# Kernel optimization log

Hardware: AMD Instinct MI355X
Metric: run time of the kernel (lower is better)

The kernel has to match this reference:

```python
import jax, jax.numpy as jnp
import numpy as np

B, C, D, H = 128, 8, 1024, 8
K_RANGE = (2, 3, 4, 5)


def setup_inputs() -> dict:
    key = jax.random.key(0)
    ks = jax.random.split(key, 10)
    s = 0.02
    return {
        "x": jax.random.normal(ks[0], (B, D), jnp.float32),
        # per-K prototype groups, shape (nb_classes, K, embed_dim) as in get_prototype_group()
        "p2": jax.random.normal(ks[1], (C, 2, D), jnp.float32),
        "p3": jax.random.normal(ks[2], (C, 3, D), jnp.float32),
        "p4": jax.random.normal(ks[3], (C, 4, D), jnp.float32),
        "p5": jax.random.normal(ks[4], (C, 5, D), jnp.float32),
        # per-class attention Block params (stacked over class axis)
        "ln_g": jnp.ones((C, D), jnp.float32),
        "ln_b": jnp.zeros((C, D), jnp.float32),
        "w_qkv": jax.random.normal(ks[5], (C, 3 * D, D), jnp.float32) * s,
        "b_qkv": jnp.zeros((C, 3 * D), jnp.float32),
        "w_proj": jax.random.normal(ks[6], (C, D, D), jnp.float32) * s,
        "b_proj": jnp.zeros((C, D), jnp.float32),
        # cls head
        "w_cls": jax.random.normal(ks[7], (C, D), jnp.float32) * s,
        "b_cls": jnp.zeros((C,), jnp.float32),
    }


def _proto_group(x, pg):
    """x: (B,D); pg: (C,K,D). Returns nearest proto (B,D), per-sample class group (B,K,D), class ids (B,)."""
    Cc, K, d = pg.shape
    flat = pg.reshape(Cc * K, d)
    # squared L2 distances (argmin identical to torch.cdist p=2 argmin)
    d2 = (jnp.sum(x * x, axis=1, keepdims=True)
          - 2.0 * (x @ flat.T)
          + jnp.sum(flat * flat, axis=1))
    idx = jnp.argmin(d2, axis=1)          # (B,)
    cls = idx // K                        # (B,)
    return flat[idx], pg[cls], cls


def _vicreg(x, nearest, proto_space, sim_c=25.0, std_c=25.0, cov_c=1.0):
    # sim: pull x toward its nearest prototype in every K-group
    repr_loss = jnp.mean((x[:, None, :] - nearest) ** 2)
    # std over batch of prototype space, unbiased var, eps=1e-4
    std = jnp.sqrt(jnp.var(proto_space, axis=0, ddof=1) + 1e-4)   # (S,D)
    std_loss = jnp.mean(jax.nn.relu(1.0 - std))
    # covariance of centered flattened prototype space
    ps = proto_space - jnp.mean(proto_space, axis=0)
    P = ps.reshape(-1, ps.shape[-1])                              # (B*S, D)
    cov = P.T @ P / (P.shape[0] - 1)
    cov_loss = ((cov ** 2).sum() - (jnp.diagonal(cov) ** 2).sum()) / ps.shape[-1]
    return sim_c * repr_loss + std_c * std_loss + cov_c * cov_loss


def _forward(x, p2, p3, p4, p5, ln_g, ln_b, w_qkv, b_qkv, w_proj, b_proj, w_cls, b_cls):
    groups = (p2, p3, p4, p5)
    nearest_list, space_list, cls = [], [], None
    for pg in groups:
        n, sp, cls = _proto_group(x, pg)   # cls kept from LAST group, as in torch code
        nearest_list.append(n)
        space_list.append(sp)
    nearest = jnp.stack(nearest_list, axis=1)     # (B, len(K_range), D)
    proto_space = jnp.concatenate(space_list, 1)  # (B, sum(K_range), D)

    vcr = _vicreg(x, nearest, proto_space)

    # per-class attention Block: LayerNorm -> MHA -> residual, vectorized over class axis c
    S = proto_space.shape[1]
    mu = proto_space.mean(-1, keepdims=True)
    var = proto_space.var(-1, keepdims=True)
    xn = (proto_space - mu) * jax.lax.rsqrt(var + 1e-5)               # (B,S,D)
    h = xn[None] * ln_g[:, None, None, :] + ln_b[:, None, None, :]    # (C,B,S,D)

    qkv = jnp.einsum('cbsd,cfd->cbsf', h, w_qkv) + b_qkv[:, None, None, :]
    dh = D // H
    qkv = qkv.reshape(C, B, S, 3, H, dh).transpose(3, 0, 1, 4, 2, 5)  # (3,C,B,H,S,dh)
    q, k, v = qkv[0] * (dh ** -0.5), qkv[1], qkv[2]
    attn = jax.nn.softmax(jnp.einsum('cbhqe,cbhke->cbhqk', q, k), axis=-1)
    o = jnp.einsum('cbhqk,cbhke->cbhqe', attn, v)                     # (C,B,H,S,dh)
    o = o.transpose(0, 1, 3, 2, 4).reshape(C, B, S, D)
    out = jnp.einsum('cbsd,ced->cbse', o, w_proj) + b_proj[:, None, None, :]
    attended = proto_space[None] + out                                # (C,B,S,D)

    # route each sample through the block of its (last-group) assigned class
    cond = attended[cls, jnp.arange(B)]                               # (B,S,D)
    cond = cond / jnp.maximum(jnp.linalg.norm(cond, axis=2, keepdims=True), 1e-12)
    pooled = cond.mean(1)                                             # (B,D)
    logits = pooled @ w_cls.T + b_cls
    return logits, vcr


def reference(x, p2, p3, p4, p5, ln_g, ln_b, w_qkv, b_qkv, w_proj, b_proj, w_cls, b_cls):
    return _forward(x, p2, p3, p4, p5, ln_g, ln_b, w_qkv, b_qkv, w_proj, b_proj, w_cls, b_cls)
```

## Files before the change

kernel.cpp:

```cpp
#include <hip/hip_runtime.h>
#include <math.h>

#define NB 128
#define ND 1024
#define NS 14
#define NDH 128

typedef float f32x4 __attribute__((ext_vector_type(4)));
typedef short bf16x8 __attribute__((ext_vector_type(8)));

__device__ __forceinline__ unsigned short f2bf(float v) {
  unsigned int u = __builtin_bit_cast(unsigned int, v);
  return (unsigned short)((u + 0x7FFFu + ((u >> 16) & 1u)) >> 16);
}
__device__ __forceinline__ float bf2f(unsigned short u) {
  return __builtin_bit_cast(float, (unsigned int)u << 16);
}

__device__ __forceinline__ void gl_lds16(const void* g, void* l) {
  __builtin_amdgcn_global_load_lds(
      (const __attribute__((address_space(1))) void*)g,
      (__attribute__((address_space(3))) void*)l, 16, 0, 0);
}

__device__ __forceinline__ void s_decomp(int s, int& g, int& k) {
  if (s < 2)      { g = 0; k = s; }
  else if (s < 5) { g = 1; k = s - 2; }
  else if (s < 9) { g = 2; k = s - 5; }
  else            { g = 3; k = s - 9; }
}
__device__ __forceinline__ const float* grp_ptr(int g, const float* p2, const float* p3,
                                                const float* p4, const float* p5) {
  return g == 0 ? p2 : g == 1 ? p3 : g == 2 ? p4 : p5;
}
__device__ __forceinline__ int grp_base(int g) { return g == 0 ? 0 : g == 1 ? 16 : g == 2 ? 40 : 72; }
__device__ __forceinline__ int grp_k(int g) { return g + 2; }

__global__ __launch_bounds__(256) void k_assign_ln(
    const float* __restrict__ x,
    const float* __restrict__ p2, const float* __restrict__ p3,
    const float* __restrict__ p4, const float* __restrict__ p5,
    const float* __restrict__ ln_g, const float* __restrict__ ln_b,
    unsigned short* __restrict__ hbf, float* __restrict__ pall,
    int* __restrict__ cls, int* __restrict__ rows_g, float* __restrict__ minv)
{
  int bid = blockIdx.x, t = threadIdx.x;
  __shared__ __align__(16) float xs[ND];
  float4* xs4 = (float4*)xs;
  if (bid < 112) {
    int r = bid;
    const float* pp; int idx;
    if (r < 16)      { pp = p2; idx = r; }
    else if (r < 40) { pp = p3; idx = r - 16; }
    else if (r < 72) { pp = p4; idx = r - 40; }
    else             { pp = p5; idx = r - 72; }
    const float4* row4 = (const float4*)(pp + (size_t)idx * ND);
    float4 v = row4[t];
    xs4[t] = v;
    float s1 = v.x + v.y + v.z + v.w;
    float s2 = v.x * v.x + v.y * v.y + v.z * v.z + v.w * v.w;
    __shared__ float ra[256], rb[256];
    ra[t] = s1; rb[t] = s2; __syncthreads();
    for (int o = 128; o > 0; o >>= 1) { if (t < o) { ra[t] += ra[t + o]; rb[t] += rb[t + o]; } __syncthreads(); }
    __shared__ float mu, rstd;
    if (t == 0) {
      float m = ra[0] * (1.f / 1024.f);
      float var = rb[0] * (1.f / 1024.f) - m * m;
      mu = m; rstd = rsqrtf(var + 1e-5f);
    }
    __syncthreads();
    ((float4*)(pall + (size_t)r * ND))[t] = xs4[t];
    float4 xv = xs4[t];
    float nx = (xv.x - mu) * rstd, ny = (xv.y - mu) * rstd,
          nz = (xv.z - mu) * rstd, nw = (xv.w - mu) * rstd;
#pragma unroll
    for (int c = 0; c < 8; ++c) {
      float4 g = ((const float4*)(ln_g + (size_t)c * ND))[t];
      float4 bb = ((const float4*)(ln_b + (size_t)c * ND))[t];
      ushort4 u;
      u.x = f2bf(nx * g.x + bb.x); u.y = f2bf(ny * g.y + bb.y);
      u.z = f2bf(nz * g.z + bb.z); u.w = f2bf(nw * g.w + bb.w);
      ((ushort4*)(hbf + ((size_t)(c * 112 + r)) * ND))[t] = u;
    }
  } else {
    int b = bid - 112;
    __shared__ float d2s[112];
    __shared__ int cls_s[4];
    const float4* xg4 = (const float4*)(x + (size_t)b * ND);
    xs4[t] = xg4[t];
    __syncthreads();
    if (t < 112) {
      const float* pp; int idx;
      if (t < 16)      { pp = p2; idx = t; }
      else if (t < 40) { pp = p3; idx = t - 16; }
      else if (t < 72) { pp = p4; idx = t - 40; }
      else             { pp = p5; idx = t - 72; }
      const float4* pr4 = (const float4*)(pp + (size_t)idx * ND);
      float acc = 0.f;
#pragma unroll 8
      for (int d = 0; d < 256; ++d) {
        float4 a = xs4[d], p = pr4[d];
        float dx = a.x - p.x, dy = a.y - p.y, dz = a.z - p.z, dw = a.w - p.w;
        acc += dx * dx + dy * dy + dz * dz + dw * dw;
      }
      d2s[t] = acc;
    }
    __syncthreads();
    if (t < 4) {
      int base = grp_base(t), kg = grp_k(t), cnt = 8 * kg;
      float mv = d2s[base]; int mi = 0;
      for (int j = 1; j < cnt; ++j) { float v = d2s[base + j]; if (v < mv) { mv = v; mi = j; } }
      int c = mi / kg;
      cls[b * 4 + t] = c; cls_s[t] = c;
      minv[b * 4 + t] = mv;
    }
    __syncthreads();
    if (t < NS) {
      int g, k; s_decomp(t, g, k);
      rows_g[b * NS + t] = grp_base(g) + cls_s[g] * grp_k(g) + k;
    }
  }
}

__global__ __launch_bounds__(128) void k_prep(
    const int* __restrict__ cls, const float* __restrict__ minv,
    int* __restrict__ counts, int* __restrict__ ccnt, int* __restrict__ order,
    float* __restrict__ scal)
{
  __shared__ int cnt_s[32];
  __shared__ int cc_s[8];
  __shared__ float red[128];
  int t = threadIdx.x;
  if (t < 32) cnt_s[t] = 0;
  if (t < 8) cc_s[t] = 0;
  if (t < 4) scal[t] = 0.f;
  __syncthreads();
  int c3;
#pragma unroll
  for (int g = 0; g < 4; ++g) {
    int c = cls[t * 4 + g];
    atomicAdd(&cnt_s[g * 8 + c], 1);
    if (g == 3) c3 = c;
  }
  int pos = atomicAdd(&cc_s[c3], 1);
  order[c3 * 128 + pos] = t;
  red[t] = minv[t * 4 + 0] + minv[t * 4 + 1] + minv[t * 4 + 2] + minv[t * 4 + 3];
  __syncthreads();
  for (int o = 64; o > 0; o >>= 1) { if (t < o) red[t] += red[t + o]; __syncthreads(); }
  if (t == 0) scal[0] = red[0];
  if (t < 32) counts[t] = cnt_s[t];
  if (t < 8) ccnt[t] = cc_s[t];
}

__global__ __launch_bounds__(256) void k_stats(
    const float* __restrict__ p2, const float* __restrict__ p3,
    const float* __restrict__ p4, const float* __restrict__ p5,
    const int* __restrict__ counts, float* __restrict__ M, float* __restrict__ scal)
{
  int idx = blockIdx.x * 256 + threadIdx.x;
  int s = idx >> 10, d = idx & 1023;
  int g, k; s_decomp(s, g, k);
  const float* pp = grp_ptr(g, p2, p3, p4, p5);
  int kg = grp_k(g);
  float vc[8], nc[8];
  float sum = 0.f, sumsq = 0.f;
#pragma unroll
  for (int c = 0; c < 8; ++c) {
    float v = pp[((size_t)(c * kg + k)) * ND + d];
    float n = (float)counts[g * 8 + c];
    vc[c] = v; nc[c] = n;
    sum += n * v; sumsq += n * v * v;
  }
  float mean = sum * (1.f / 128.f);
  float var = (sumsq - 128.f * mean * mean) * (1.f / 127.f);
  float sd = sqrtf(var + 1e-4f);
#pragma unroll
  for (int c = 0; c < 8; ++c)
    M[((size_t)(s * 8 + c)) * ND + d] = sqrtf(nc[c] * (1.f / 1791.f)) * (vc[c] - mean);
  float part = fmaxf(1.f - sd, 0.f);
  __shared__ float red[256];
  red[threadIdx.x] = part; __syncthreads();
  for (int o = 128; o > 0; o >>= 1) { if (threadIdx.x < o) red[threadIdx.x] += red[threadIdx.x + o]; __syncthreads(); }
  if (threadIdx.x == 0) atomicAdd(&scal[1], red[0]);
}

__global__ __launch_bounds__(128) void k_gramdiag(const float* __restrict__ M, float* __restrict__ scal)
{
  __shared__ float mi[ND];
  __shared__ float red[128];
  int bid = blockIdx.x, t = threadIdx.x;
  if (bid < 112) {
    for (int d = t; d < ND; d += 128) mi[d] = M[(size_t)bid * ND + d];
    __syncthreads();
    float p = 0.f;
    if (t < 112) {
      const float* mj = M + (size_t)t * ND;
      float acc = 0.f;
      for (int d = 0; d < ND; ++d) acc += mi[d] * mj[d];
      p = acc * acc;
    }
    red[t] = p; __syncthreads();
    for (int o = 64; o > 0; o >>= 1) { if (t < o) red[t] += red[t + o]; __syncthreads(); }
    if (t == 0) atomicAdd(&scal[2], red[0]);
  } else {
    int d = (bid - 112) * 128 + t;
    float tsum = 0.f;
    for (int r = 0; r < 112; ++r) { float v = M[(size_t)r * ND + d]; tsum += v * v; }
    red[t] = tsum * tsum; __syncthreads();
    for (int o = 64; o > 0; o >>= 1) { if (t < o) red[t] += red[t + o]; __syncthreads(); }
    if (t == 0) atomicAdd(&scal[3], red[0]);
  }
}

__global__ __launch_bounds__(128) void k_qkv_mfma(
    const unsigned short* __restrict__ hbf, const float* __restrict__ w_qkv,
    const float* __restrict__ b_qkv, unsigned short* __restrict__ qkv_bf)
{
  __shared__ __align__(16) float Wl[32 * 128];
  __shared__ __align__(16) unsigned short Hl[112 * 128];
  int c = blockIdx.y;
  int nb0 = blockIdx.x * 32;
  int t = threadIdx.x, lane = t & 63, wv = t >> 6;
  const float* W = w_qkv + ((size_t)c * 3072 + nb0) * ND;
  const unsigned short* H = hbf + (size_t)c * 112 * ND;

  const char* wsrc[8]; char* wdst[8];
#pragma unroll
  for (int j = 0; j < 8; ++j) {
    int n = (wv * 8 + j) * 2 + (lane >> 5);
    int cbs = ((lane & 31) * 16) ^ ((n & 15) << 5);
    wsrc[j] = (const char*)(W + (size_t)n * ND) + cbs;
    wdst[j] = (char*)Wl + (wv * 8 + j) * 1024;
  }
  const char* hsrc[14]; char* hdst[14];
#pragma unroll
  for (int j = 0; j < 14; ++j) {
    int r = (wv * 14 + j) * 4 + (lane >> 4);
    int cbs = ((lane & 15) * 16) ^ ((r & 15) << 4);
    hsrc[j] = (const char*)(H + (size_t)r * ND) + cbs;
    hdst[j] = (char*)Hl + (wv * 14 + j) * 1024;
  }

  f32x4 acc[7] = {};
  int r16 = lane & 15, q = lane >> 4;
  const char* wrow = (const char*)Wl + (wv * 16 + r16) * 512;
  int swq = r16 << 5, swa = r16 << 4;

  for (int kt = 0; kt < ND; kt += 128) {
    __syncthreads();
#pragma unroll
    for (int j = 0; j < 8; ++j) gl_lds16(wsrc[j] + (size_t)kt * 4, wdst[j]);
#pragma unroll
    for (int j = 0; j < 14; ++j) gl_lds16(hsrc[j] + (size_t)kt * 2, hdst[j]);
    __syncthreads();
#pragma unroll
    for (int kk4 = 0; kk4 < 4; ++kk4) {
      int o = (kk4 * 128 + q * 32) ^ swq;
      float4 w0 = *(const float4*)(wrow + o);
      float4 w1 = *(const float4*)(wrow + o + 16);
      bf16x8 bv;
      bv[0] = (short)f2bf(w0.x); bv[1] = (short)f2bf(w0.y);
      bv[2] = (short)f2bf(w0.z); bv[3] = (short)f2bf(w0.w);
      bv[4] = (short)f2bf(w1.x); bv[5] = (short)f2bf(w1.y);
      bv[6] = (short)f2bf(w1.z); bv[7] = (short)f2bf(w1.w);
      int oa = (kk4 * 64 + q * 16) ^ swa;
#pragma unroll
      for (int m = 0; m < 7; ++m) {
        bf16x8 av = *(const bf16x8*)((const char*)Hl + (m * 16 + r16) * 256 + oa);
        acc[m] = __builtin_amdgcn_mfma_f32_16x16x32_bf16(av, bv, acc[m], 0, 0, 0);
      }
    }
  }
  int col = nb0 + wv * 16 + r16;
  float bq = b_qkv[(size_t)c * 3072 + col];
  int rbase = q * 4;
#pragma unroll
  for (int m = 0; m < 7; ++m)
#pragma unroll
    for (int r = 0; r < 4; ++r)
      qkv_bf[((size_t)c * 112 + m * 16 + rbase + r) * 3072 + col] = f2bf(acc[m][r] + bq);
}

__global__ __launch_bounds__(256) void k_attn(
    const unsigned short* __restrict__ qkv_bf, const int* __restrict__ cls,
    const int* __restrict__ rows_g, unsigned short* __restrict__ obf)
{
  __shared__ __align__(16) float qs[NS * NDH], ks2[NS * NDH], vs[NS * NDH];
  __shared__ float sc[NS * NS];
  __shared__ int rg[NS];
  int h = blockIdx.x, b = blockIdx.y, t = threadIdx.x;
  if (t < NS) rg[t] = rows_g[b * NS + t];
  __syncthreads();
  int cp = cls[b * 4 + 3];
  const float scale = 0.08838834764831843f;
  for (int i = t; i < NS * 64; i += 256) {
    int s = i >> 6, e2 = (i & 63) * 2;
    size_t base = ((size_t)cp * 112 + rg[s]) * 3072 + h * NDH + e2;
    unsigned int uq = *(const unsigned int*)&qkv_bf[base];
    unsigned int uk = *(const unsigned int*)&qkv_bf[base + 1024];
    unsigned int uv = *(const unsigned int*)&qkv_bf[base + 2048];
    qs[s * NDH + e2]      = bf2f((unsigned short)uq) * scale;
    qs[s * NDH + e2 + 1]  = bf2f((unsigned short)(uq >> 16)) * scale;
    ks2[s * NDH + e2]     = bf2f((unsigned short)uk);
    ks2[s * NDH + e2 + 1] = bf2f((unsigned short)(uk >> 16));
    vs[s * NDH + e2]      = bf2f((unsigned short)uv);
    vs[s * NDH + e2 + 1]  = bf2f((unsigned short)(uv >> 16));
  }
  __syncthreads();
  if (t < NS * NS) {
    int si = t / NS, sj = t - (t / NS) * NS;
    const float4* qa = (const float4*)&qs[si * NDH];
    const float4* kb = (const float4*)&ks2[sj * NDH];
    float acc = 0.f;
#pragma unroll 8
    for (int e4 = 0; e4 < 32; ++e4) {
      float4 a = qa[e4], k4 = kb[e4];
      acc += a.x * k4.x + a.y * k4.y + a.z * k4.z + a.w * k4.w;
    }
    sc[t] = acc;
  }
  __syncthreads();
  if (t < NS) {
    float m = -1e30f;
    for (int j = 0; j < NS; ++j) m = fmaxf(m, sc[t * NS + j]);
    float e_[NS]; float sum = 0.f;
    for (int j = 0; j < NS; ++j) { float e = expf(sc[t * NS + j] - m); e_[j] = e; sum += e; }
    float inv = 1.f / sum;
    for (int j = 0; j < NS; ++j) sc[t * NS + j] = e_[j] * inv;
  }
  __syncthreads();
  for (int i = t; i < NS * 32; i += 256) {
    int s = i >> 5, e4 = i & 31;
    float4 a = {0.f, 0.f, 0.f, 0.f};
#pragma unroll
    for (int j = 0; j < NS; ++j) {
      float w = sc[s * NS + j];
      float4 v4 = ((const float4*)&vs[j * NDH])[e4];
      a.x += w * v4.x; a.y += w * v4.y; a.z += w * v4.z; a.w += w * v4.w;
    }
    ushort4 u; u.x = f2bf(a.x); u.y = f2bf(a.y); u.z = f2bf(a.z); u.w = f2bf(a.w);
    ((ushort4*)&obf[((size_t)b * NS + s) * ND + h * NDH])[e4] = u;
  }
}

__global__ __launch_bounds__(256) void k_proj_mfma(
    const unsigned short* __restrict__ obf, const int* __restrict__ order,
    const int* __restrict__ ccnt, const int* __restrict__ rows_g,
    const float* __restrict__ w_proj, const float* __restrict__ b_proj,
    const float* __restrict__ pall, float* __restrict__ att)
{
  int c = blockIdx.y >> 3, ch = blockIdx.y & 7;
  int cnt = ccnt[c];
  int nb = cnt - ch * 16;
  if (nb <= 0) return;
  if (nb > 16) nb = 16;
  __shared__ __align__(16) float Wl[32 * 128];
  __shared__ __align__(16) unsigned short Al[224 * 128];
  __shared__ int sid_s[16];
  int t = threadIdx.x, lane = t & 63, wv = t >> 6;
  if (t < 16) sid_s[t] = order[c * 128 + ch * 16 + ((t < nb) ? t : 0)];
  __syncthreads();
  int nb0 = blockIdx.x * 32;
  const float* W = w_proj + ((size_t)c * ND + nb0) * ND;

  const char* wsrc[4]; char* wdst[4];
#pragma unroll
  for (int j = 0; j < 4; ++j) {
    int n = (wv * 4 + j) * 2 + (lane >> 5);
    int cbs = ((lane & 31) * 16) ^ ((n & 15) << 5);
    wsrc[j] = (const char*)(W + (size_t)n * ND) + cbs;
    wdst[j] = (char*)Wl + (wv * 4 + j) * 1024;
  }
  const char* asrc[14]; char* adst[14];
#pragma unroll
  for (int j = 0; j < 14; ++j) {
    int r = (wv * 14 + j) * 4 + (lane >> 4);
    int cbs = ((lane & 15) * 16) ^ ((r & 15) << 4);
    int si = r / 14, s = r - si * 14;
    asrc[j] = (const char*)(obf + ((size_t)sid_s[si] * NS + s) * ND) + cbs;
    adst[j] = (char*)Al + (wv * 14 + j) * 1024;
  }

  f32x4 acc[7] = {};
  int r16 = lane & 15, q = lane >> 4;
  int colh = wv & 1, rowh = wv >> 1;
  const char* wrow = (const char*)Wl + (colh * 16 + r16) * 512;
  int swq = r16 << 5, swa = r16 << 4;

  for (int kt = 0; kt < ND; kt += 128) {
    __syncthreads();
#pragma unroll
    for (int j = 0; j < 4; ++j) gl_lds16(wsrc[j] + (size_t)kt * 4, wdst[j]);
#pragma unroll
    for (int j = 0; j < 14; ++j) gl_lds16(asrc[j] + (size_t)kt * 2, adst[j]);
    __syncthreads();
#pragma unroll
    for (int kk4 = 0; kk4 < 4; ++kk4) {
      int o = (kk4 * 128 + q * 32) ^ swq;
      float4 w0 = *(const float4*)(wrow + o);
      float4 w1 = *(const float4*)(wrow + o + 16);
      bf16x8 bv;
      bv[0] = (short)f2bf(w0.x); bv[1] = (short)f2bf(w0.y);
      bv[2] = (short)f2bf(w0.z); bv[3] = (short)f2bf(w0.w);
      bv[4] = (short)f2bf(w1.x); bv[5] = (short)f2bf(w1.y);
      bv[6] = (short)f2bf(w1.z); bv[7] = (short)f2bf(w1.w);
      int oa = (kk4 * 64 + q * 16) ^ swa;
#pragma unroll
      for (int m = 0; m < 7; ++m) {
        int row = rowh * 112 + m * 16 + r16;
        bf16x8 av = *(const bf16x8*)((const char*)Al + row * 256 + oa);
        acc[m] = __builtin_amdgcn_mfma_f32_16x16x32_bf16(av, bv, acc[m], 0, 0, 0);
      }
    }
  }
  int col = nb0 + colh * 16 + r16;
  float bp = b_proj[(size_t)c * ND + col];
  int rbase = q * 4;
#pragma unroll
  for (int m = 0; m < 7; ++m)
#pragma unroll
    for (int r = 0; r < 4; ++r) {
      int row = rowh * 112 + m * 16 + rbase + r;
      int si = row / 14, s = row - si * 14;
      if (si < nb) {
        int b = sid_s[si];
        float res = pall[(size_t)rows_g[b * NS + s] * ND + col];
        att[((size_t)b * NS + s) * ND + col] = acc[m][r] + bp + res;
      }
    }
}

__global__ __launch_bounds__(256) void k_final(
    const float* __restrict__ att, const float* __restrict__ w_cls,
    const float* __restrict__ b_cls, const float* __restrict__ scal,
    float* __restrict__ out)
{
  int b = blockIdx.x, t = threadIdx.x;
  __shared__ __align__(16) float as[NS * ND];
  __shared__ float wred[NS][4];
  __shared__ float inv[NS];
  __shared__ __align__(16) float pooled[ND];
  int lane = t & 63, w = t >> 6;
#pragma unroll
  for (int s = 0; s < NS; ++s) {
    float4 v = ((const float4*)(att + ((size_t)b * NS + s) * ND))[t];
    ((float4*)&as[s * ND])[t] = v;
    float p = v.x * v.x + v.y * v.y + v.z * v.z + v.w * v.w;
#pragma unroll
    for (int o = 32; o > 0; o >>= 1) p += __shfl_xor(p, o, 64);
    if (lane == 0) wred[s][w] = p;
  }
  __syncthreads();
  if (t < NS) {
    float s2 = wred[t][0] + wred[t][1] + wred[t][2] + wred[t][3];
    inv[t] = 1.f / fmaxf(sqrtf(s2), 1e-12f);
  }
  __syncthreads();
  float4 pa = {0.f, 0.f, 0.f, 0.f};
#pragma unroll
  for (int s = 0; s < NS; ++s) {
    float iv = inv[s];
    float4 v = ((const float4*)&as[s * ND])[t];
    pa.x += iv * v.x; pa.y += iv * v.y; pa.z += iv * v.z; pa.w += iv * v.w;
  }
  const float k14 = 1.f / 14.f;
  pa.x *= k14; pa.y *= k14; pa.z *= k14; pa.w *= k14;
  ((float4*)pooled)[t] = pa;
  __syncthreads();
  int c = t >> 5, l = t & 31;
  float acc = 0.f;
#pragma unroll
  for (int k = 0; k < 8; ++k) {
    int i4 = l + k * 32;
    float4 p4 = ((const float4*)pooled)[i4];
    float4 wc = ((const float4*)(w_cls + (size_t)c * ND))[i4];
    acc += p4.x * wc.x + p4.y * wc.y + p4.z * wc.z + p4.w * wc.w;
  }
  for (int o = 16; o > 0; o >>= 1) acc += __shfl_down(acc, o, 32);
  if (l == 0) out[b * 8 + c] = acc + b_cls[c];
  if (b == 0 && t == 0) {
    float repr = scal[0] * (1.f / (128.f * 4.f * 1024.f));
    float stdl = scal[1] * (1.f / 14336.f);
    float covl = (scal[2] - scal[3]) * (1.f / 1024.f);
    out[1024] = 25.f * repr + 25.f * stdl + covl;
  }
}

extern "C" void kernel_launch(void* const* d_in, const int* in_sizes, int n_in,
                              void* d_out, int out_size, void* d_ws, size_t ws_size,
                              hipStream_t stream) {
  const float* x      = (const float*)d_in[0];
  const float* p2     = (const float*)d_in[1];
  const float* p3     = (const float*)d_in[2];
  const float* p4     = (const float*)d_in[3];
  const float* p5     = (const float*)d_in[4];
  const float* ln_g   = (const float*)d_in[5];
  const float* ln_b   = (const float*)d_in[6];
  const float* w_qkv  = (const float*)d_in[7];
  const float* b_qkv  = (const float*)d_in[8];
  const float* w_proj = (const float*)d_in[9];
  const float* b_proj = (const float*)d_in[10];
  const float* w_cls  = (const float*)d_in[11];
  const float* b_cls  = (const float*)d_in[12];
  float* out = (float*)d_out;
  char* ws = (char*)d_ws;

  float* scal   = (float*)(ws + 0);
  int*   counts = (int*)(ws + 64);
  int*   ccnt   = (int*)(ws + 192);
  int*   cls    = (int*)(ws + 256);
  int*   rows_g = (int*)(ws + 2304);
  int*   order  = (int*)(ws + 9472);
  float* minv   = (float*)(ws + 13568);
  float* pall   = (float*)(ws + 16384);
  unsigned short* hbf  = (unsigned short*)(ws + 475136);
  unsigned short* qkvb = (unsigned short*)(ws + 2310144);
  unsigned short* obf  = (unsigned short*)(ws + 9191424);
  float* att    = (float*)(ws + 12861440);
  float* M      = (float*)(ws + 20201472);

  k_assign_ln<<<240, 256, 0, stream>>>(x, p2, p3, p4, p5, ln_g, ln_b, hbf, pall, cls, rows_g, minv);
  k_qkv_mfma<<<dim3(96, 8), 128, 0, stream>>>(hbf, w_qkv, b_qkv, qkvb);
  k_prep<<<1, 128, 0, stream>>>(cls, minv, counts, ccnt, order, scal);
  k_stats<<<56, 256, 0, stream>>>(p2, p3, p4, p5, counts, M, scal);
  k_gramdiag<<<120, 128, 0, stream>>>(M, scal);
  k_attn<<<dim3(8, 128), 256, 0, stream>>>(qkvb, cls, rows_g, obf);
  k_proj_mfma<<<dim3(32, 64), 256, 0, stream>>>(obf, order, ccnt, rows_g, w_proj, b_proj, pall, att);
  k_final<<<128, 256, 0, stream>>>(att, w_cls, b_cls, scal, out);
}
```

Measured before the change: 136.0 us.

## Store GEMM operands in MFMA fragment order and load directly from global memory

The LayerNorm output and the attention output are now written in a pre-swizzled layout that matches the MFMA 16x16x32 operand fragment order. This lets the QKV and projection GEMMs drop LDS staging and barriers and read operands straight from global/L2. The projection kernel now computes 64 output columns per block with 14 accumulators, halving the grid, and weight conversion uses the packed bf16 convert instruction. k_gramdiag also gets float4 vectorized loads. The trade-off is the loss of explicit LDS reuse, relying on cache for operands that are reread across blocks and waves, plus higher register pressure.

```diff
diff --git a/kernel.cpp b/kernel.cpp
--- a/kernel.cpp
+++ b/kernel.cpp
@@ -8,6 +8,7 @@
 
 typedef float f32x4 __attribute__((ext_vector_type(4)));
 typedef short bf16x8 __attribute__((ext_vector_type(8)));
+typedef unsigned int u32x4 __attribute__((ext_vector_type(4)));
 
 __device__ __forceinline__ unsigned short f2bf(float v) {
   unsigned int u = __builtin_bit_cast(unsigned int, v);
@@ -17,10 +18,14 @@
   return __builtin_bit_cast(float, (unsigned int)u << 16);
 }
 
-__device__ __forceinline__ void gl_lds16(const void* g, void* l) {
-  __builtin_amdgcn_global_load_lds(
-      (const __attribute__((address_space(1))) void*)g,
-      (__attribute__((address_space(3))) void*)l, 16, 0, 0);
+__device__ __forceinline__ bf16x8 pack_bv(float4 w0, float4 w1) {
+  unsigned int u0, u1, u2, u3;
+  asm("v_cvt_pk_bf16_f32 %0, %1, %2" : "=v"(u0) : "v"(w0.x), "v"(w0.y));
+  asm("v_cvt_pk_bf16_f32 %0, %1, %2" : "=v"(u1) : "v"(w0.z), "v"(w0.w));
+  asm("v_cvt_pk_bf16_f32 %0, %1, %2" : "=v"(u2) : "v"(w1.x), "v"(w1.y));
+  asm("v_cvt_pk_bf16_f32 %0, %1, %2" : "=v"(u3) : "v"(w1.z), "v"(w1.w));
+  u32x4 u = {u0, u1, u2, u3};
+  return __builtin_bit_cast(bf16x8, u);
 }
 
 __device__ __forceinline__ void s_decomp(int s, int& g, int& k) {
@@ -41,7 +46,7 @@
     const float* __restrict__ p2, const float* __restrict__ p3,
     const float* __restrict__ p4, const float* __restrict__ p5,
     const float* __restrict__ ln_g, const float* __restrict__ ln_b,
-    unsigned short* __restrict__ hbf, float* __restrict__ pall,
+    unsigned short* __restrict__ hbf2, float* __restrict__ pall,
     int* __restrict__ cls, int* __restrict__ rows_g, float* __restrict__ minv)
 {
   int bid = blockIdx.x, t = threadIdx.x;
@@ -73,6 +78,10 @@
     float4 xv = xs4[t];
     float nx = (xv.x - mu) * rstd, ny = (xv.y - mu) * rstd,
           nz = (xv.z - mu) * rstd, nw = (xv.w - mu) * rstd;
+    int d0 = t * 4;
+    int m = r >> 4, rr = r & 15;
+    int kblk = d0 >> 5, qq = (d0 >> 3) & 3, e0 = d0 & 7;
+    size_t fidx = (((size_t)kblk * 7 + m) * 64 + qq * 16 + rr) * 8 + e0;
 #pragma unroll
     for (int c = 0; c < 8; ++c) {
       float4 g = ((const float4*)(ln_g + (size_t)c * ND))[t];
@@ -80,7 +89,7 @@
       ushort4 u;
       u.x = f2bf(nx * g.x + bb.x); u.y = f2bf(ny * g.y + bb.y);
       u.z = f2bf(nz * g.z + bb.z); u.w = f2bf(nw * g.w + bb.w);
-      ((ushort4*)(hbf + ((size_t)(c * 112 + r)) * ND))[t] = u;
+      *(ushort4*)&hbf2[(size_t)c * 114688 + fidx] = u;
     }
   } else {
     int b = bid - 112;
@@ -186,17 +195,23 @@
 
 __global__ __launch_bounds__(128) void k_gramdiag(const float* __restrict__ M, float* __restrict__ scal)
 {
-  __shared__ float mi[ND];
+  __shared__ __align__(16) float mi[ND];
   __shared__ float red[128];
   int bid = blockIdx.x, t = threadIdx.x;
   if (bid < 112) {
-    for (int d = t; d < ND; d += 128) mi[d] = M[(size_t)bid * ND + d];
+    float4* mi4 = (float4*)mi;
+    const float4* src4 = (const float4*)(M + (size_t)bid * ND);
+    for (int d = t; d < 256; d += 128) mi4[d] = src4[d];
     __syncthreads();
     float p = 0.f;
     if (t < 112) {
-      const float* mj = M + (size_t)t * ND;
+      const float4* mj4 = (const float4*)(M + (size_t)t * ND);
       float acc = 0.f;
-      for (int d = 0; d < ND; ++d) acc += mi[d] * mj[d];
+#pragma unroll 8
+      for (int d = 0; d < 256; ++d) {
+        float4 a = mi4[d], b = mj4[d];
+        acc += a.x * b.x + a.y * b.y + a.z * b.z + a.w * b.w;
+      }
       p = acc * acc;
     }
     red[t] = p; __syncthreads();
@@ -213,65 +228,28 @@
 }
 
 __global__ __launch_bounds__(128) void k_qkv_mfma(
-    const unsigned short* __restrict__ hbf, const float* __restrict__ w_qkv,
+    const unsigned short* __restrict__ hbf2, const float* __restrict__ w_qkv,
     const float* __restrict__ b_qkv, unsigned short* __restrict__ qkv_bf)
 {
-  __shared__ __align__(16) float Wl[32 * 128];
-  __shared__ __align__(16) unsigned short Hl[112 * 128];
   int c = blockIdx.y;
-  int nb0 = blockIdx.x * 32;
   int t = threadIdx.x, lane = t & 63, wv = t >> 6;
-  const float* W = w_qkv + ((size_t)c * 3072 + nb0) * ND;
-  const unsigned short* H = hbf + (size_t)c * 112 * ND;
-
-  const char* wsrc[8]; char* wdst[8];
-#pragma unroll
-  for (int j = 0; j < 8; ++j) {
-    int n = (wv * 8 + j) * 2 + (lane >> 5);
-    int cbs = ((lane & 31) * 16) ^ ((n & 15) << 5);
-    wsrc[j] = (const char*)(W + (size_t)n * ND) + cbs;
-    wdst[j] = (char*)Wl + (wv * 8 + j) * 1024;
-  }
-  const char* hsrc[14]; char* hdst[14];
-#pragma unroll
-  for (int j = 0; j < 14; ++j) {
-    int r = (wv * 14 + j) * 4 + (lane >> 4);
-    int cbs = ((lane & 15) * 16) ^ ((r & 15) << 4);
-    hsrc[j] = (const char*)(H + (size_t)r * ND) + cbs;
-    hdst[j] = (char*)Hl + (wv * 14 + j) * 1024;
-  }
-
+  int r16 = lane & 15, q = lane >> 4;
+  int col = blockIdx.x * 32 + wv * 16 + r16;
+  const float* Wp = w_qkv + ((size_t)c * 3072 + col) * ND + q * 8;
+  const unsigned short* Hp = hbf2 + (size_t)c * 114688 + lane * 8;
   f32x4 acc[7] = {};
-  int r16 = lane & 15, q = lane >> 4;
-  const char* wrow = (const char*)Wl + (wv * 16 + r16) * 512;
-  int swq = r16 << 5, swa = r16 << 4;
-
-  for (int kt = 0; kt < ND; kt += 128) {
-    __syncthreads();
-#pragma unroll
-    for (int j = 0; j < 8; ++j) gl_lds16(wsrc[j] + (size_t)kt * 4, wdst[j]);
-#pragma unroll
-    for (int j = 0; j < 14; ++j) gl_lds16(hsrc[j] + (size_t)kt * 2, hdst[j]);
-    __syncthreads();
-#pragma unroll
-    for (int kk4 = 0; kk4 < 4; ++kk4) {
-      int o = (kk4 * 128 + q * 32) ^ swq;
-      float4 w0 = *(const float4*)(wrow + o);
-      float4 w1 = *(const float4*)(wrow + o + 16);
-      bf16x8 bv;
-      bv[0] = (short)f2bf(w0.x); bv[1] = (short)f2bf(w0.y);
-      bv[2] = (short)f2bf(w0.z); bv[3] = (short)f2bf(w0.w);
-      bv[4] = (short)f2bf(w1.x); bv[5] = (short)f2bf(w1.y);
-      bv[6] = (short)f2bf(w1.z); bv[7] = (short)f2bf(w1.w);
-      int oa = (kk4 * 64 + q * 16) ^ swa;
-#pragma unroll
-      for (int m = 0; m < 7; ++m) {
-        bf16x8 av = *(const bf16x8*)((const char*)Hl + (m * 16 + r16) * 256 + oa);
-        acc[m] = __builtin_amdgcn_mfma_f32_16x16x32_bf16(av, bv, acc[m], 0, 0, 0);
-      }
-    }
-  }
-  int col = nb0 + wv * 16 + r16;
+#pragma unroll 2
+  for (int kb = 0; kb < 32; ++kb) {
+    float4 w0 = *(const float4*)(Wp + kb * 32);
+    float4 w1 = *(const float4*)(Wp + kb * 32 + 4);
+    bf16x8 bv = pack_bv(w0, w1);
+    const unsigned short* hk = Hp + kb * 3584;
+#pragma unroll
+    for (int m = 0; m < 7; ++m) {
+      bf16x8 av = *(const bf16x8*)(hk + m * 512);
+      acc[m] = __builtin_amdgcn_mfma_f32_16x16x32_bf16(av, bv, acc[m], 0, 0, 0);
+    }
+  }
   float bq = b_qkv[(size_t)c * 3072 + col];
   int rbase = q * 4;
 #pragma unroll
@@ -283,7 +261,7 @@
 
 __global__ __launch_bounds__(256) void k_attn(
     const unsigned short* __restrict__ qkv_bf, const int* __restrict__ cls,
-    const int* __restrict__ rows_g, unsigned short* __restrict__ obf)
+    const int* __restrict__ rows_g, unsigned short* __restrict__ obf2)
 {
   __shared__ __align__(16) float qs[NS * NDH], ks2[NS * NDH], vs[NS * NDH];
   __shared__ float sc[NS * NS];
@@ -338,13 +316,15 @@
       float4 v4 = ((const float4*)&vs[j * NDH])[e4];
       a.x += w * v4.x; a.y += w * v4.y; a.z += w * v4.z; a.w += w * v4.w;
     }
+    int d = h * NDH + e4 * 4;
+    int kblk = d >> 5, qq = (d >> 3) & 3, e0 = d & 7;
     ushort4 u; u.x = f2bf(a.x); u.y = f2bf(a.y); u.z = f2bf(a.z); u.w = f2bf(a.w);
-    ((ushort4*)&obf[((size_t)b * NS + s) * ND + h * NDH])[e4] = u;
+    *(ushort4*)&obf2[(size_t)b * 14336 + kblk * 448 + s * 32 + qq * 8 + e0] = u;
   }
 }
 
 __global__ __launch_bounds__(256) void k_proj_mfma(
-    const unsigned short* __restrict__ obf, const int* __restrict__ order,
+    const unsigned short* __restrict__ obf2, const int* __restrict__ order,
     const int* __restrict__ ccnt, const int* __restrict__ rows_g,
     const float* __restrict__ w_proj, const float* __restrict__ b_proj,
     const float* __restrict__ pall, float* __restrict__ att)
@@ -354,73 +334,40 @@
   int nb = cnt - ch * 16;
   if (nb <= 0) return;
   if (nb > 16) nb = 16;
-  __shared__ __align__(16) float Wl[32 * 128];
-  __shared__ __align__(16) unsigned short Al[224 * 128];
   __shared__ int sid_s[16];
   int t = threadIdx.x, lane = t & 63, wv = t >> 6;
   if (t < 16) sid_s[t] = order[c * 128 + ch * 16 + ((t < nb) ? t : 0)];
   __syncthreads();
-  int nb0 = blockIdx.x * 32;
-  const float* W = w_proj + ((size_t)c * ND + nb0) * ND;
-
-  const char* wsrc[4]; char* wdst[4];
-#pragma unroll
-  for (int j = 0; j < 4; ++j) {
-    int n = (wv * 4 + j) * 2 + (lane >> 5);
-    int cbs = ((lane & 31) * 16) ^ ((n & 15) << 5);
-    wsrc[j] = (const char*)(W + (size_t)n * ND) + cbs;
-    wdst[j] = (char*)Wl + (wv * 4 + j) * 1024;
-  }
-  const char* asrc[14]; char* adst[14];
-#pragma unroll
-  for (int j = 0; j < 14; ++j) {
-    int r = (wv * 14 + j) * 4 + (lane >> 4);
-    int cbs = ((lane & 15) * 16) ^ ((r & 15) << 4);
-    int si = r / 14, s = r - si * 14;
-    asrc[j] = (const char*)(obf + ((size_t)sid_s[si] * NS + s) * ND) + cbs;
-    adst[j] = (char*)Al + (wv * 14 + j) * 1024;
-  }
-
-  f32x4 acc[7] = {};
   int r16 = lane & 15, q = lane >> 4;
-  int colh = wv & 1, rowh = wv >> 1;
-  const char* wrow = (const char*)Wl + (colh * 16 + r16) * 512;
-  int swq = r16 << 5, swa = r16 << 4;
-
-  for (int kt = 0; kt < ND; kt += 128) {
-    __syncthreads();
-#pragma unroll
-    for (int j = 0; j < 4; ++j) gl_lds16(wsrc[j] + (size_t)kt * 4, wdst[j]);
-#pragma unroll
-    for (int j = 0; j < 14; ++j) gl_lds16(asrc[j] + (size_t)kt * 2, adst[j]);
-    __syncthreads();
-#pragma unroll
-    for (int kk4 = 0; kk4 < 4; ++kk4) {
-      int o = (kk4 * 128 + q * 32) ^ swq;
-      float4 w0 = *(const float4*)(wrow + o);
-      float4 w1 = *(const float4*)(wrow + o + 16);
-      bf16x8 bv;
-      bv[0] = (short)f2bf(w0.x); bv[1] = (short)f2bf(w0.y);
-      bv[2] = (short)f2bf(w0.z); bv[3] = (short)f2bf(w0.w);
-      bv[4] = (short)f2bf(w1.x); bv[5] = (short)f2bf(w1.y);
-      bv[6] = (short)f2bf(w1.z); bv[7] = (short)f2bf(w1.w);
-      int oa = (kk4 * 64 + q * 16) ^ swa;
-#pragma unroll
-      for (int m = 0; m < 7; ++m) {
-        int row = rowh * 112 + m * 16 + r16;
-        bf16x8 av = *(const bf16x8*)((const char*)Al + row * 256 + oa);
-        acc[m] = __builtin_amdgcn_mfma_f32_16x16x32_bf16(av, bv, acc[m], 0, 0, 0);
-      }
-    }
-  }
-  int col = nb0 + colh * 16 + r16;
+  int col = blockIdx.x * 64 + wv * 16 + r16;
+  const float* Wp = w_proj + ((size_t)c * ND + col) * ND + q * 8;
+  const unsigned short* ap[14];
+#pragma unroll
+  for (int m = 0; m < 14; ++m) {
+    int row = m * 16 + r16;
+    int si = row / 14, s = row - si * 14;
+    ap[m] = obf2 + (size_t)sid_s[si] * 14336 + s * 32 + q * 8;
+  }
+  f32x4 acc[14] = {};
+#pragma unroll 2
+  for (int kb = 0; kb < 32; ++kb) {
+    float4 w0 = *(const float4*)(Wp + kb * 32);
+    float4 w1 = *(const float4*)(Wp + kb * 32 + 4);
+    bf16x8 bv = pack_bv(w0, w1);
+    int ko = kb * 448;
+#pragma unroll
+    for (int m = 0; m < 14; ++m) {
+      bf16x8 av = *(const bf16x8*)(ap[m] + ko);
+      acc[m] = __builtin_amdgcn_mfma_f32_16x16x32_bf16(av, bv, acc[m], 0, 0, 0);
+    }
+  }
   float bp = b_proj[(size_t)c * ND + col];
   int rbase = q * 4;
 #pragma unroll
-  for (int m = 0; m < 7; ++m)
+  for (int m = 0; m < 14; ++m)
 #pragma unroll
     for (int r = 0; r < 4; ++r) {
-      int row = rowh * 112 + m * 16 + rbase + r;
+      int row = m * 16 + rbase + r;
       int si = row / 14, s = row - si * 14;
       if (si < nb) {
         int b = sid_s[si];
@@ -513,18 +460,18 @@
   int*   order  = (int*)(ws + 9472);
   float* minv   = (float*)(ws + 13568);
   float* pall   = (float*)(ws + 16384);
-  unsigned short* hbf  = (unsigned short*)(ws + 475136);
+  unsigned short* hbf2 = (unsigned short*)(ws + 475136);
   unsigned short* qkvb = (unsigned short*)(ws + 2310144);
-  unsigned short* obf  = (unsigned short*)(ws + 9191424);
+  unsigned short* obf2 = (unsigned short*)(ws + 9191424);
   float* att    = (float*)(ws + 12861440);
   float* M      = (float*)(ws + 20201472);
 
-  k_assign_ln<<<240, 256, 0, stream>>>(x, p2, p3, p4, p5, ln_g, ln_b, hbf, pall, cls, rows_g, minv);
-  k_qkv_mfma<<<dim3(96, 8), 128, 0, stream>>>(hbf, w_qkv, b_qkv, qkvb);
+  k_assign_ln<<<240, 256, 0, stream>>>(x, p2, p3, p4, p5, ln_g, ln_b, hbf2, pall, cls, rows_g, minv);
+  k_qkv_mfma<<<dim3(96, 8), 128, 0, stream>>>(hbf2, w_qkv, b_qkv, qkvb);
   k_prep<<<1, 128, 0, stream>>>(cls, minv, counts, ccnt, order, scal);
   k_stats<<<56, 256, 0, stream>>>(p2, p3, p4, p5, counts, M, scal);
   k_gramdiag<<<120, 128, 0, stream>>>(M, scal);
-  k_attn<<<dim3(8, 128), 256, 0, stream>>>(qkvb, cls, rows_g, obf);
-  k_proj_mfma<<<dim3(32, 64), 256, 0, stream>>>(obf, order, ccnt, rows_g, w_proj, b_proj, pall, att);
+  k_attn<<<dim3(8, 128), 256, 0, stream>>>(qkvb, cls, rows_g, obf2);
+  k_proj_mfma<<<dim3(16, 64), 256, 0, stream>>>(obf2, order, ccnt, rows_g, w_proj, b_proj, pall, att);
   k_final<<<128, 256, 0, stream>>>(att, w_cls, b_cls, scal, out);
 }
```

Result: slower. 196.8 us (+44.7%).

## Split-K QKV GEMM with MFMA-fragment-ordered LN output and separate reduce

Applied to the files above, without the earlier changes.

The LayerNorm kernel now writes its bf16 output in an MFMA fragment-ordered layout, so the QKV GEMM can load A fragments directly from global memory without LDS staging. The QKV GEMM is split along K into 4 slices, with more blocks of 4 waves each, and a separate reduce kernel sums the partial results and adds the bias. This raises parallelism and removes LDS sync overhead, at the cost of extra fp32 partial-sum traffic and one more launch. It also uses the packed v_cvt_pk_bf16_f32 instruction for weight conversion and vectorises the gramdiag dot products with float4 loads.

```diff
diff --git a/kernel.cpp b/kernel.cpp
--- a/kernel.cpp
+++ b/kernel.cpp
@@ -8,6 +8,7 @@
 
 typedef float f32x4 __attribute__((ext_vector_type(4)));
 typedef short bf16x8 __attribute__((ext_vector_type(8)));
+typedef unsigned int u32x4 __attribute__((ext_vector_type(4)));
 
 __device__ __forceinline__ unsigned short f2bf(float v) {
   unsigned int u = __builtin_bit_cast(unsigned int, v);
@@ -21,6 +22,16 @@
   __builtin_amdgcn_global_load_lds(
       (const __attribute__((address_space(1))) void*)g,
       (__attribute__((address_space(3))) void*)l, 16, 0, 0);
+}
+
+__device__ __forceinline__ bf16x8 pack_bv(float4 w0, float4 w1) {
+  unsigned int u0, u1, u2, u3;
+  asm("v_cvt_pk_bf16_f32 %0, %1, %2" : "=v"(u0) : "v"(w0.x), "v"(w0.y));
+  asm("v_cvt_pk_bf16_f32 %0, %1, %2" : "=v"(u1) : "v"(w0.z), "v"(w0.w));
+  asm("v_cvt_pk_bf16_f32 %0, %1, %2" : "=v"(u2) : "v"(w1.x), "v"(w1.y));
+  asm("v_cvt_pk_bf16_f32 %0, %1, %2" : "=v"(u3) : "v"(w1.z), "v"(w1.w));
+  u32x4 u = {u0, u1, u2, u3};
+  return __builtin_bit_cast(bf16x8, u);
 }
 
 __device__ __forceinline__ void s_decomp(int s, int& g, int& k) {
@@ -41,7 +52,7 @@
     const float* __restrict__ p2, const float* __restrict__ p3,
     const float* __restrict__ p4, const float* __restrict__ p5,
     const float* __restrict__ ln_g, const float* __restrict__ ln_b,
-    unsigned short* __restrict__ hbf, float* __restrict__ pall,
+    unsigned short* __restrict__ hbf2, float* __restrict__ pall,
     int* __restrict__ cls, int* __restrict__ rows_g, float* __restrict__ minv)
 {
   int bid = blockIdx.x, t = threadIdx.x;
@@ -73,6 +84,10 @@
     float4 xv = xs4[t];
     float nx = (xv.x - mu) * rstd, ny = (xv.y - mu) * rstd,
           nz = (xv.z - mu) * rstd, nw = (xv.w - mu) * rstd;
+    int d0 = t * 4;
+    int m = r >> 4, rr = r & 15;
+    int kblk = d0 >> 5, qq = (d0 >> 3) & 3, e0 = d0 & 7;
+    size_t fidx = (size_t)kblk * 3584 + m * 512 + (qq * 16 + rr) * 8 + e0;
 #pragma unroll
     for (int c = 0; c < 8; ++c) {
       float4 g = ((const float4*)(ln_g + (size_t)c * ND))[t];
@@ -80,7 +95,7 @@
       ushort4 u;
       u.x = f2bf(nx * g.x + bb.x); u.y = f2bf(ny * g.y + bb.y);
       u.z = f2bf(nz * g.z + bb.z); u.w = f2bf(nw * g.w + bb.w);
-      ((ushort4*)(hbf + ((size_t)(c * 112 + r)) * ND))[t] = u;
+      *(ushort4*)&hbf2[(size_t)c * 114688 + fidx] = u;
     }
   } else {
     int b = bid - 112;
@@ -186,17 +201,23 @@
 
 __global__ __launch_bounds__(128) void k_gramdiag(const float* __restrict__ M, float* __restrict__ scal)
 {
-  __shared__ float mi[ND];
+  __shared__ __align__(16) float mi[ND];
   __shared__ float red[128];
   int bid = blockIdx.x, t = threadIdx.x;
   if (bid < 112) {
-    for (int d = t; d < ND; d += 128) mi[d] = M[(size_t)bid * ND + d];
+    float4* mi4 = (float4*)mi;
+    const float4* src4 = (const float4*)(M + (size_t)bid * ND);
+    for (int d = t; d < 256; d += 128) mi4[d] = src4[d];
     __syncthreads();
     float p = 0.f;
     if (t < 112) {
-      const float* mj = M + (size_t)t * ND;
+      const float4* mj4 = (const float4*)(M + (size_t)t * ND);
       float acc = 0.f;
-      for (int d = 0; d < ND; ++d) acc += mi[d] * mj[d];
+#pragma unroll 8
+      for (int d = 0; d < 256; ++d) {
+        float4 a = mi4[d], b = mj4[d];
+        acc += a.x * b.x + a.y * b.y + a.z * b.z + a.w * b.w;
+      }
       p = acc * acc;
     }
     red[t] = p; __syncthreads();
@@ -212,73 +233,61 @@
   }
 }
 
-__global__ __launch_bounds__(128) void k_qkv_mfma(
-    const unsigned short* __restrict__ hbf, const float* __restrict__ w_qkv,
-    const float* __restrict__ b_qkv, unsigned short* __restrict__ qkv_bf)
-{
-  __shared__ __align__(16) float Wl[32 * 128];
-  __shared__ __align__(16) unsigned short Hl[112 * 128];
-  int c = blockIdx.y;
-  int nb0 = blockIdx.x * 32;
-  int t = threadIdx.x, lane = t & 63, wv = t >> 6;
-  const float* W = w_qkv + ((size_t)c * 3072 + nb0) * ND;
-  const unsigned short* H = hbf + (size_t)c * 112 * ND;
-
-  const char* wsrc[8]; char* wdst[8];
-#pragma unroll
-  for (int j = 0; j < 8; ++j) {
-    int n = (wv * 8 + j) * 2 + (lane >> 5);
-    int cbs = ((lane & 31) * 16) ^ ((n & 15) << 5);
-    wsrc[j] = (const char*)(W + (size_t)n * ND) + cbs;
-    wdst[j] = (char*)Wl + (wv * 8 + j) * 1024;
-  }
-  const char* hsrc[14]; char* hdst[14];
-#pragma unroll
-  for (int j = 0; j < 14; ++j) {
-    int r = (wv * 14 + j) * 4 + (lane >> 4);
-    int cbs = ((lane & 15) * 16) ^ ((r & 15) << 4);
-    hsrc[j] = (const char*)(H + (size_t)r * ND) + cbs;
-    hdst[j] = (char*)Hl + (wv * 14 + j) * 1024;
-  }
-
+__global__ __launch_bounds__(256) void k_qkv_gemm(
+    const unsigned short* __restrict__ hbf2, const float* __restrict__ w_qkv,
+    float* __restrict__ psum)
+{
+  int c = blockIdx.y, s = blockIdx.z;
+  int t = threadIdx.x, lane = t & 63, w = t >> 6;
+  int cb = blockIdx.x * 4 + w;
+  int r16 = lane & 15, q = lane >> 4;
+  int col = cb * 16 + r16;
+  const float* Wp = w_qkv + ((size_t)c * 3072 + col) * ND + s * 256 + q * 8;
+  const unsigned short* Hp = hbf2 + (size_t)c * 114688 + (size_t)(s * 8) * 3584 + lane * 8;
   f32x4 acc[7] = {};
+#pragma unroll
+  for (int i = 0; i < 8; ++i) {
+    float4 w0 = *(const float4*)(Wp + i * 32);
+    float4 w1 = *(const float4*)(Wp + i * 32 + 4);
+    bf16x8 bv = pack_bv(w0, w1);
+    const unsigned short* hk = Hp + (size_t)i * 3584;
+#pragma unroll
+    for (int m = 0; m < 7; ++m) {
+      bf16x8 av = *(const bf16x8*)(hk + m * 512);
+      acc[m] = __builtin_amdgcn_mfma_f32_16x16x32_bf16(av, bv, acc[m], 0, 0, 0);
+    }
+  }
+  float* po = psum + ((size_t)(s * 1536 + c * 192 + cb)) * 1792 + lane * 4;
+#pragma unroll
+  for (int m = 0; m < 7; ++m)
+    *(f32x4*)(po + m * 256) = acc[m];
+}
+
+__global__ __launch_bounds__(256) void k_qkv_reduce(
+    const float* __restrict__ psum, const float* __restrict__ b_qkv,
+    unsigned short* __restrict__ qkv_bf)
+{
+  const size_t sp = 2752512;
+  int idx = blockIdx.x * 256 + threadIdx.x;
+  int lane = idx & 63;
+  int wsl = idx >> 6;
+  int m = wsl % 7;
+  int cc = wsl / 7;
+  int cb = cc % 192, c = cc / 192;
+  size_t fo = (size_t)cc * 1792 + m * 256 + lane * 4;
+  float4 a0 = *(const float4*)(psum + fo);
+  float4 a1 = *(const float4*)(psum + sp + fo);
+  float4 a2 = *(const float4*)(psum + 2 * sp + fo);
+  float4 a3 = *(const float4*)(psum + 3 * sp + fo);
   int r16 = lane & 15, q = lane >> 4;
-  const char* wrow = (const char*)Wl + (wv * 16 + r16) * 512;
-  int swq = r16 << 5, swa = r16 << 4;
-
-  for (int kt = 0; kt < ND; kt += 128) {
-    __syncthreads();
-#pragma unroll
-    for (int j = 0; j < 8; ++j) gl_lds16(wsrc[j] + (size_t)kt * 4, wdst[j]);
-#pragma unroll
-    for (int j = 0; j < 14; ++j) gl_lds16(hsrc[j] + (size_t)kt * 2, hdst[j]);
-    __syncthreads();
-#pragma unroll
-    for (int kk4 = 0; kk4 < 4; ++kk4) {
-      int o = (kk4 * 128 + q * 32) ^ swq;
-      float4 w0 = *(const float4*)(wrow + o);
-      float4 w1 = *(const float4*)(wrow + o + 16);
-      bf16x8 bv;
-      bv[0] = (short)f2bf(w0.x); bv[1] = (short)f2bf(w0.y);
-      bv[2] = (short)f2bf(w0.z); bv[3] = (short)f2bf(w0.w);
-      bv[4] = (short)f2bf(w1.x); bv[5] = (short)f2bf(w1.y);
-      bv[6] = (short)f2bf(w1.z); bv[7] = (short)f2bf(w1.w);
-      int oa = (kk4 * 64 + q * 16) ^ swa;
-#pragma unroll
-      for (int m = 0; m < 7; ++m) {
-        bf16x8 av = *(const bf16x8*)((const char*)Hl + (m * 16 + r16) * 256 + oa);
-        acc[m] = __builtin_amdgcn_mfma_f32_16x16x32_bf16(av, bv, acc[m], 0, 0, 0);
-      }
-    }
-  }
-  int col = nb0 + wv * 16 + r16;
-  float bq = b_qkv[(size_t)c * 3072 + col];
-  int rbase = q * 4;
-#pragma unroll
-  for (int m = 0; m < 7; ++m)
-#pragma unroll
-    for (int r = 0; r < 4; ++r)
-      qkv_bf[((size_t)c * 112 + m * 16 + rbase + r) * 3072 + col] = f2bf(acc[m][r] + bq);
+  int col = cb * 16 + r16;
+  float bq = b_qkv[c * 3072 + col];
+  int row0 = m * 16 + q * 4;
+  size_t ob = ((size_t)c * 112 + row0) * 3072 + col;
+  qkv_bf[ob]        = f2bf(a0.x + a1.x + a2.x + a3.x + bq);
+  qkv_bf[ob + 3072] = f2bf(a0.y + a1.y + a2.y + a3.y + bq);
+  qkv_bf[ob + 6144] = f2bf(a0.z + a1.z + a2.z + a3.z + bq);
+  qkv_bf[ob + 9216] = f2bf(a0.w + a1.w + a2.w + a3.w + bq);
 }
 
 __global__ __launch_bounds__(256) void k_attn(
@@ -399,11 +408,7 @@
       int o = (kk4 * 128 + q * 32) ^ swq;
       float4 w0 = *(const float4*)(wrow + o);
       float4 w1 = *(const float4*)(wrow + o + 16);
-      bf16x8 bv;
-      bv[0] = (short)f2bf(w0.x); bv[1] = (short)f2bf(w0.y);
-      bv[2] = (short)f2bf(w0.z); bv[3] = (short)f2bf(w0.w);
-      bv[4] = (short)f2bf(w1.x); bv[5] = (short)f2bf(w1.y);
-      bv[6] = (short)f2bf(w1.z); bv[7] = (short)f2bf(w1.w);
+      bf16x8 bv = pack_bv(w0, w1);
       int oa = (kk4 * 64 + q * 16) ^ swa;
 #pragma unroll
       for (int m = 0; m < 7; ++m) {
@@ -513,14 +518,16 @@
   int*   order  = (int*)(ws + 9472);
   float* minv   = (float*)(ws + 13568);
   float* pall   = (float*)(ws + 16384);
-  unsigned short* hbf  = (unsigned short*)(ws + 475136);
+  unsigned short* hbf2 = (unsigned short*)(ws + 475136);
   unsigned short* qkvb = (unsigned short*)(ws + 2310144);
-  unsigned short* obf  = (unsigned short*)(ws + 9191424);
-  float* att    = (float*)(ws + 12861440);
-  float* M      = (float*)(ws + 20201472);
-
-  k_assign_ln<<<240, 256, 0, stream>>>(x, p2, p3, p4, p5, ln_g, ln_b, hbf, pall, cls, rows_g, minv);
-  k_qkv_mfma<<<dim3(96, 8), 128, 0, stream>>>(hbf, w_qkv, b_qkv, qkvb);
+  unsigned short* obf  = (unsigned short*)(ws + 7815168);
+  float* att    = (float*)(ws + 11485184);
+  float* M      = (float*)(ws + 18825216);
+  float* psum   = (float*)(ws + 19283968);
+
+  k_assign_ln<<<240, 256, 0, stream>>>(x, p2, p3, p4, p5, ln_g, ln_b, hbf2, pall, cls, rows_g, minv);
+  k_qkv_gemm<<<dim3(48, 8, 4), 256, 0, stream>>>(hbf2, w_qkv, psum);
+  k_qkv_reduce<<<2688, 256, 0, stream>>>(psum, b_qkv, qkvb);
   k_prep<<<1, 128, 0, stream>>>(cls, minv, counts, ccnt, order, scal);
   k_stats<<<56, 256, 0, stream>>>(p2, p3, p4, p5, counts, M, scal);
   k_gramdiag<<<120, 128, 0, stream>>>(M, scal);
```

After: 144.5 us. +6.2%, slower.
